# Kernel tuning notes

Measured on AMD Instinct MI355X. Metric: run time of the kernel, lower is better.

## Reference

```python
import jax, jax.numpy as jnp
import numpy as np

B, N, D, E = 4, 16384, 128, 1048576  # batch, nodes/graph, hidden, total edges


def setup_inputs() -> dict:
    key = jax.random.key(0)
    k0, k1, k2, k3, k4, k5, k6 = jax.random.split(key, 7)
    x = jax.random.normal(k0, (B, N, D), dtype=jnp.float32)
    W = jax.random.normal(k1, (D, D), dtype=jnp.float32) * 0.05  # 'random_normal' init
    b = jax.random.normal(k2, (D,), dtype=jnp.float32) * 0.05
    edge_b = jax.random.randint(k3, (E,), 0, B, dtype=jnp.int32)
    edge_row = jax.random.randint(k4, (E,), 0, N, dtype=jnp.int32)
    edge_col = jax.random.randint(k5, (E,), 0, N, dtype=jnp.int32)
    edge_vals = jax.random.uniform(k6, (E,), dtype=jnp.float32)
    return {"x": x, "W": W, "b": b, "edge_b": edge_b, "edge_row": edge_row,
            "edge_col": edge_col, "edge_vals": edge_vals, "k": 2}


def reference(x, W, b, edge_b, edge_row, edge_col, edge_vals, k):
    # adj is a batched sparse [B, N, N]; edges stored as (batch, row, col, val) COO.
    seg_row = edge_b * N + edge_row  # flattened destination id in [0, B*N)
    # in_degrees = sum_j |adj[b, i, j]|
    deg = jax.ops.segment_sum(jnp.abs(edge_vals), seg_row, num_segments=B * N)
    deg = deg.reshape(B, N)
    norm = jnp.power(deg + 1e-6, -0.5)[..., None]          # [B, N, 1]
    norm_k = jnp.power(norm, k)                             # computed but unused (faithful to source)
    support = jnp.einsum('bnd,de->bne', x, W)               # x @ W
    y = (support * norm).reshape(B * N, D)                  # pre-normalized features
    # SpMM: out[b, i] = sum_{(b,i,j)} adj_val * y[b, j]
    msgs = y[edge_b * N + edge_col] * edge_vals[:, None]    # [E, D] gather + scale
    agg = jax.ops.segment_sum(msgs, seg_row, num_segments=B * N).reshape(B, N, D)
    return jax.nn.relu(agg * norm + b)
```

## Files before the change

kernel.cpp:

```cpp
#include <hip/hip_runtime.h>
#include <stdint.h>

#define B_ 4
#define N_ 16384
#define D_ 128
#define E_ 1048576
#define BN_ 65536
#define NBKT 256
#define NBLK 256
#define CAP  6144
#define CAPQ 1536

typedef __attribute__((ext_vector_type(8))) short short8;
typedef __attribute__((ext_vector_type(4))) float floatx4;

static constexpr size_t OFF_Y      = 0;
static constexpr size_t OFF_PACK1  = 16777216;
static constexpr size_t OFF_GBKT   = OFF_PACK1 + 12582912;
static constexpr size_t OFF_NORM   = OFF_GBKT + 1024;
static constexpr size_t OFF_ROWST  = OFF_NORM + 262144;
static constexpr size_t OFF_WH     = OFF_ROWST + 262144;
static constexpr size_t OFF_WL     = OFF_WH + 32768;

__device__ __forceinline__ uint32_t rne16(uint32_t u) {
    return (u + 0x7FFFu + ((u >> 16) & 1u)) >> 16;
}
__device__ __forceinline__ void bf16split(float f, uint16_t& h, uint16_t& l) {
    uint32_t hb = rne16(__float_as_uint(f));
    h = (uint16_t)hb;
    float r = f - __uint_as_float(hb << 16);
    l = (uint16_t)rne16(__float_as_uint(r));
}

__global__ __launch_bounds__(1024, 2) void k_scatter(const int* __restrict__ eb,
                                                     const int* __restrict__ er,
                                                     const int* __restrict__ ec,
                                                     const float* __restrict__ ev,
                                                     const float* __restrict__ Wg,
                                                     uint32_t* __restrict__ gbkt,
                                                     uint2* __restrict__ pack1,
                                                     uint16_t* __restrict__ WhG,
                                                     uint16_t* __restrict__ WlG) {
    __shared__ uint32_t h[NBKT];
    int t = threadIdx.x;
    if (t < NBKT) h[t] = 0;
    if (blockIdx.x < 16) {
        int g = blockIdx.x * 1024 + t;
        float w = Wg[g];
        uint16_t hh, ll;
        bf16split(w, hh, ll);
        int k = g >> 7, n = g & 127;
        int o = ((k >> 3) * 128 + n) * 8 + (k & 7);
        WhG[o] = hh;
        WlG[o] = ll;
    }
    __syncthreads();
    int vbase = blockIdx.x * 1024 + t;
    int4   b4 = ((const int4*)eb)[vbase];
    int4   r4 = ((const int4*)er)[vbase];
    int4   c4 = ((const int4*)ec)[vbase];
    float4 v4 = ((const float4*)ev)[vbase];
    uint32_t k0 = (uint32_t)(b4.x * N_ + r4.x);
    uint32_t k1 = (uint32_t)(b4.y * N_ + r4.y);
    uint32_t k2 = (uint32_t)(b4.z * N_ + r4.z);
    uint32_t k3 = (uint32_t)(b4.w * N_ + r4.w);
    atomicAdd(&h[k0 >> 8], 1u);
    atomicAdd(&h[k1 >> 8], 1u);
    atomicAdd(&h[k2 >> 8], 1u);
    atomicAdd(&h[k3 >> 8], 1u);
    __syncthreads();
    if (t < NBKT) {
        uint32_t c = h[t];
        uint32_t base = c ? atomicAdd(&gbkt[t], c) : 0u;
        h[t] = base;
    }
    __syncthreads();
    {
        uint32_t off = atomicAdd(&h[k0 >> 8], 1u);
        pack1[(size_t)(k0 >> 8) * CAP + off] =
            make_uint2(((k0 & 255u) << 14) | (uint32_t)c4.x, __float_as_uint(v4.x));
    }
    {
        uint32_t off = atomicAdd(&h[k1 >> 8], 1u);
        pack1[(size_t)(k1 >> 8) * CAP + off] =
            make_uint2(((k1 & 255u) << 14) | (uint32_t)c4.y, __float_as_uint(v4.y));
    }
    {
        uint32_t off = atomicAdd(&h[k2 >> 8], 1u);
        pack1[(size_t)(k2 >> 8) * CAP + off] =
            make_uint2(((k2 & 255u) << 14) | (uint32_t)c4.z, __float_as_uint(v4.z));
    }
    {
        uint32_t off = atomicAdd(&h[k3 >> 8], 1u);
        pack1[(size_t)(k3 >> 8) * CAP + off] =
            make_uint2(((k3 & 255u) << 14) | (uint32_t)c4.w, __float_as_uint(v4.w));
    }
}

__global__ __launch_bounds__(1024) void k_degsort(const uint32_t* __restrict__ gbkt,
                                                  const uint2* __restrict__ pack1,
                                                  float* __restrict__ norm,
                                                  uint32_t* __restrict__ rowst) {
    __shared__ float    dsum[NBKT];
    __shared__ uint32_t cnt[NBKT];
    __shared__ uint32_t scn[NBKT];
    int t = threadIdx.x;
    int bkt = blockIdx.x;
    if (t < NBKT) { dsum[t] = 0.f; cnt[t] = 0; }
    __syncthreads();
    uint32_t n = gbkt[bkt];
    size_t bstart = (size_t)bkt * CAP;
    for (uint32_t i = t; i < n; i += 1024) {
        uint2 p = pack1[bstart + i];
        uint32_t nl = p.x >> 14;
        atomicAdd(&cnt[nl], 1u);
        atomicAdd(&dsum[nl], fabsf(__uint_as_float(p.y)));
    }
    __syncthreads();
    if (t < NBKT) scn[t] = cnt[t];
    __syncthreads();
    for (int off = 1; off < NBKT; off <<= 1) {
        uint32_t a = 0;
        if (t < NBKT && t >= off) a = scn[t - off];
        __syncthreads();
        if (t < NBKT) scn[t] += a;
        __syncthreads();
    }
    if (t < NBKT) {
        norm[bkt * NBKT + t] = rsqrtf(dsum[t] + 1e-6f);
        rowst[bkt * NBKT + t] = scn[t] - cnt[t];
    }
}

__global__ __launch_bounds__(256) void k_matmul_mfma(const float* __restrict__ x,
                                                     const uint16_t* __restrict__ WhG,
                                                     const uint16_t* __restrict__ WlG,
                                                     const float* __restrict__ norm,
                                                     uint32_t* __restrict__ ybf) {
    __shared__ short WhS[16384];
    __shared__ short WlS[16384];
    __shared__ short XhS[4096];
    __shared__ short XlS[4096];
    __shared__ float normS[32];
    int tid = threadIdx.x;
    int row0 = blockIdx.x * 32;

    {
        const uint4* whg = (const uint4*)WhG;
        const uint4* wlg = (const uint4*)WlG;
        uint4* whs = (uint4*)WhS;
        uint4* wls = (uint4*)WlS;
#pragma unroll
        for (int i = 0; i < 8; ++i) {
            whs[i * 256 + tid] = whg[i * 256 + tid];
            wls[i * 256 + tid] = wlg[i * 256 + tid];
        }
    }
#pragma unroll
    for (int cc = 0; cc < 2; ++cc) {
        int c = cc * 256 + tid;
        int m = c & 31, kk = c >> 5;
        const float4* xp = (const float4*)(x + (size_t)(row0 + m) * D_ + kk * 8);
        float4 f0 = xp[0], f1 = xp[1];
        union { short8 v; uint16_t s[8]; } uh, ul;
        bf16split(f0.x, uh.s[0], ul.s[0]); bf16split(f0.y, uh.s[1], ul.s[1]);
        bf16split(f0.z, uh.s[2], ul.s[2]); bf16split(f0.w, uh.s[3], ul.s[3]);
        bf16split(f1.x, uh.s[4], ul.s[4]); bf16split(f1.y, uh.s[5], ul.s[5]);
        bf16split(f1.z, uh.s[6], ul.s[6]); bf16split(f1.w, uh.s[7], ul.s[7]);
        ((short8*)XhS)[c] = uh.v;
        ((short8*)XlS)[c] = ul.v;
    }
    if (tid < 32) normS[tid] = norm[row0 + tid];
    __syncthreads();

    int lane = tid & 63;
    int wv = tid >> 6;
    int quad = lane >> 4;
    int l15 = lane & 15;
    int wcol0 = wv * 32;
    floatx4 acc[2][2] = {};
    const short8* Xh8 = (const short8*)XhS;
    const short8* Xl8 = (const short8*)XlS;
    const short8* Wh8 = (const short8*)WhS;
    const short8* Wl8 = (const short8*)WlS;
#pragma unroll
    for (int ks = 0; ks < 4; ++ks) {
        int kkq = ks * 4 + quad;
        short8 ah0 = Xh8[kkq * 32 + l15];
        short8 ah1 = Xh8[kkq * 32 + 16 + l15];
        short8 al0 = Xl8[kkq * 32 + l15];
        short8 al1 = Xl8[kkq * 32 + 16 + l15];
        short8 bh0 = Wh8[kkq * 128 + wcol0 + l15];
        short8 bh1 = Wh8[kkq * 128 + wcol0 + 16 + l15];
        short8 bl0 = Wl8[kkq * 128 + wcol0 + l15];
        short8 bl1 = Wl8[kkq * 128 + wcol0 + 16 + l15];
        acc[0][0] = __builtin_amdgcn_mfma_f32_16x16x32_bf16(ah0, bh0, acc[0][0], 0, 0, 0);
        acc[0][1] = __builtin_amdgcn_mfma_f32_16x16x32_bf16(ah0, bh1, acc[0][1], 0, 0, 0);
        acc[1][0] = __builtin_amdgcn_mfma_f32_16x16x32_bf16(ah1, bh0, acc[1][0], 0, 0, 0);
        acc[1][1] = __builtin_amdgcn_mfma_f32_16x16x32_bf16(ah1, bh1, acc[1][1], 0, 0, 0);
        acc[0][0] = __builtin_amdgcn_mfma_f32_16x16x32_bf16(ah0, bl0, acc[0][0], 0, 0, 0);
        acc[0][1] = __builtin_amdgcn_mfma_f32_16x16x32_bf16(ah0, bl1, acc[0][1], 0, 0, 0);
        acc[1][0] = __builtin_amdgcn_mfma_f32_16x16x32_bf16(ah1, bl0, acc[1][0], 0, 0, 0);
        acc[1][1] = __builtin_amdgcn_mfma_f32_16x16x32_bf16(ah1, bl1, acc[1][1], 0, 0, 0);
        acc[0][0] = __builtin_amdgcn_mfma_f32_16x16x32_bf16(al0, bh0, acc[0][0], 0, 0, 0);
        acc[0][1] = __builtin_amdgcn_mfma_f32_16x16x32_bf16(al0, bh1, acc[0][1], 0, 0, 0);
        acc[1][0] = __builtin_amdgcn_mfma_f32_16x16x32_bf16(al1, bh0, acc[1][0], 0, 0, 0);
        acc[1][1] = __builtin_amdgcn_mfma_f32_16x16x32_bf16(al1, bh1, acc[1][1], 0, 0, 0);
    }

#pragma unroll
    for (int rt = 0; rt < 2; ++rt) {
#pragma unroll
        for (int ct = 0; ct < 2; ++ct) {
            floatx4 v = acc[rt][ct];
            int rbase = rt * 16 + quad * 4;
            int cp = (wcol0 + ct * 16) / 2 + (l15 >> 1);
#pragma unroll
            for (int r = 0; r < 4; ++r) {
                float mine = v[r] * normS[rbase + r];
                float oth = __shfl_xor(mine, 1, 64);
                uint32_t a = __float_as_uint((lane & 1) ? oth : mine);
                uint32_t b = __float_as_uint((lane & 1) ? mine : oth);
                uint32_t packed = rne16(a) | (rne16(b) << 16);
                bool doit = ((lane & 1) == 0) ? (r < 2) : (r >= 2);
                if (doit)
                    ybf[(size_t)(row0 + rbase + r) * 64 + cp] = packed;
            }
        }
    }
}

__device__ __forceinline__ void fma8(float* acc, float v, uint4 u) {
    acc[0] = fmaf(v, __uint_as_float(u.x << 16), acc[0]);
    acc[1] = fmaf(v, __uint_as_float(u.x & 0xFFFF0000u), acc[1]);
    acc[2] = fmaf(v, __uint_as_float(u.y << 16), acc[2]);
    acc[3] = fmaf(v, __uint_as_float(u.y & 0xFFFF0000u), acc[3]);
    acc[4] = fmaf(v, __uint_as_float(u.z << 16), acc[4]);
    acc[5] = fmaf(v, __uint_as_float(u.z & 0xFFFF0000u), acc[5]);
    acc[6] = fmaf(v, __uint_as_float(u.w << 16), acc[6]);
    acc[7] = fmaf(v, __uint_as_float(u.w & 0xFFFF0000u), acc[7]);
}

__global__ __launch_bounds__(512, 8) void k_spmm(const uint32_t* __restrict__ gbkt,
                                                 const uint2* __restrict__ pack1,
                                                 const uint32_t* __restrict__ rowst,
                                                 const uint4* __restrict__ y4,
                                                 const float* __restrict__ norm,
                                                 const float* __restrict__ bias,
                                                 float* __restrict__ out) {
    __shared__ uint2    srt[CAPQ];
    __shared__ uint32_t rs[65];
    __shared__ uint32_t rcur[64];
    int t = threadIdx.x;
    int blk = blockIdx.x;
    int xcd = blk & 7;
    int batch = xcd & 3;
    int qhi = xcd >> 2;
    int j = blk >> 3;
    int quarter = qhi * 2 + (j & 1);
    int bkt = batch * 64 + (j >> 1);
    int nbase = quarter * 64;
    uint32_t n = gbkt[bkt];
    if (t < 64) { rs[t] = rowst[bkt * NBKT + nbase + t]; rcur[t] = 0; }
    if (t == 64) rs[64] = (quarter == 3) ? n : rowst[bkt * NBKT + nbase + 64];
    __syncthreads();
    uint32_t qbase = rs[0];
    size_t base = (size_t)bkt * CAP;
    for (uint32_t i = t; i < n; i += 512) {
        uint2 p = pack1[base + i];
        uint32_t nl = p.x >> 14;
        if ((int)(nl >> 6) == quarter) {
            uint32_t loc = nl & 63;
            uint32_t pos = rs[loc] - qbase + atomicAdd(&rcur[loc], 1u);
            srt[pos] = p;
        }
    }
    __syncthreads();

    int wv = t >> 6;
    int lane = t & 63;
    int esub = lane >> 4;
    int chunk = lane & 15;
    uint32_t colbase = (uint32_t)batch << 14;
#pragma unroll 1
    for (int i = 0; i < 8; ++i) {
        int nl = wv * 8 + i;
        uint32_t e = rs[nl] - qbase;
        uint32_t end = rs[nl + 1] - qbase;
        float acc[8] = {0.f,0.f,0.f,0.f,0.f,0.f,0.f,0.f};
        for (; e + 16 <= end; e += 16) {
            uint2 pa = srt[e + esub];
            uint2 pb = srt[e + 4 + esub];
            uint2 pc = srt[e + 8 + esub];
            uint2 pd = srt[e + 12 + esub];
            uint4 ua = y4[(size_t)(colbase | (pa.x & 0x3FFFu)) * 16 + chunk];
            uint4 ub = y4[(size_t)(colbase | (pb.x & 0x3FFFu)) * 16 + chunk];
            uint4 uc = y4[(size_t)(colbase | (pc.x & 0x3FFFu)) * 16 + chunk];
            uint4 ud = y4[(size_t)(colbase | (pd.x & 0x3FFFu)) * 16 + chunk];
            fma8(acc, __uint_as_float(pa.y), ua);
            fma8(acc, __uint_as_float(pb.y), ub);
            fma8(acc, __uint_as_float(pc.y), uc);
            fma8(acc, __uint_as_float(pd.y), ud);
        }
        for (; e + 4 <= end; e += 4) {
            uint2 p = srt[e + esub];
            uint4 u = y4[(size_t)(colbase | (p.x & 0x3FFFu)) * 16 + chunk];
            fma8(acc, __uint_as_float(p.y), u);
        }
        if (e < end) {
            uint32_t idx = e + esub;
            bool act = idx < end;
            uint2 p = srt[act ? idx : (end - 1)];
            uint4 u = y4[(size_t)(colbase | (p.x & 0x3FFFu)) * 16 + chunk];
            float v = act ? __uint_as_float(p.y) : 0.f;
            fma8(acc, v, u);
        }
#pragma unroll
        for (int jj = 0; jj < 8; ++jj) {
            acc[jj] += __shfl_xor(acc[jj], 16, 64);
            acc[jj] += __shfl_xor(acc[jj], 32, 64);
        }
        if (esub < 2) {
            int node = bkt * NBKT + nbase + nl;
            float nm = norm[node];
            float4 bb = ((const float4*)bias)[chunk * 2 + esub];
            float4 o;
            o.x = fmaxf(fmaf(acc[esub * 4 + 0], nm, bb.x), 0.f);
            o.y = fmaxf(fmaf(acc[esub * 4 + 1], nm, bb.y), 0.f);
            o.z = fmaxf(fmaf(acc[esub * 4 + 2], nm, bb.z), 0.f);
            o.w = fmaxf(fmaf(acc[esub * 4 + 3], nm, bb.w), 0.f);
            ((float4*)out)[(size_t)node * 32 + chunk * 2 + esub] = o;
        }
    }
}

extern "C" void kernel_launch(void* const* d_in, const int* in_sizes, int n_in,
                              void* d_out, int out_size, void* d_ws, size_t ws_size,
                              hipStream_t stream) {
    const float* x  = (const float*)d_in[0];
    const float* W  = (const float*)d_in[1];
    const float* bi = (const float*)d_in[2];
    const int* eb   = (const int*)d_in[3];
    const int* er   = (const int*)d_in[4];
    const int* ec   = (const int*)d_in[5];
    const float* ev = (const float*)d_in[6];
    float* out = (float*)d_out;

    char* ws = (char*)d_ws;
    uint32_t* ybf    = (uint32_t*)(ws + OFF_Y);
    uint2*    pack1  = (uint2*)(ws + OFF_PACK1);
    uint32_t* gbkt   = (uint32_t*)(ws + OFF_GBKT);
    float*    norm   = (float*)(ws + OFF_NORM);
    uint32_t* rowst  = (uint32_t*)(ws + OFF_ROWST);
    uint16_t* WhG    = (uint16_t*)(ws + OFF_WH);
    uint16_t* WlG    = (uint16_t*)(ws + OFF_WL);

    hipMemsetAsync(gbkt, 0, NBKT * sizeof(uint32_t), stream);
    k_scatter<<<NBLK, 1024, 0, stream>>>(eb, er, ec, ev, W, gbkt, pack1, WhG, WlG);
    k_degsort<<<NBKT, 1024, 0, stream>>>(gbkt, pack1, norm, rowst);
    k_matmul_mfma<<<BN_ / 32, 256, 0, stream>>>(x, WhG, WlG, norm, ybf);
    k_spmm   <<<1024, 512, 0, stream>>>(gbkt, pack1, rowst, (const uint4*)ybf, norm, bi, out);
}
```

Measured before the change: 181.3 us.

## Sort edges by row once in degsort and read sorted edges globally in SpMM

The per-row counting sort of each bucket's edges moves into the degree kernel, which stages it in LDS (48KB) and writes the sorted bucket back to global memory in place. The SpMM kernel no longer rescans the whole bucket four times, once per quarter block, to build an LDS-sorted copy. It reads edges straight from global memory at the row offsets. This removes redundant global reads and LDS atomics in SpMM and shrinks its LDS use, which may raise occupancy. In exchange, edge reads in the inner loop become global loads instead of LDS loads, and degsort does an extra read and write pass. Bounds checks against CAP are also added.

```diff
diff --git a/kernel.cpp b/kernel.cpp
--- a/kernel.cpp
+++ b/kernel.cpp
@@ -9,7 +9,6 @@
 #define NBKT 256
 #define NBLK 256
 #define CAP  6144
-#define CAPQ 1536
 
 typedef __attribute__((ext_vector_type(8))) short short8;
 typedef __attribute__((ext_vector_type(4))) float floatx4;
@@ -77,38 +76,45 @@
     __syncthreads();
     {
         uint32_t off = atomicAdd(&h[k0 >> 8], 1u);
-        pack1[(size_t)(k0 >> 8) * CAP + off] =
-            make_uint2(((k0 & 255u) << 14) | (uint32_t)c4.x, __float_as_uint(v4.x));
+        if (off < CAP)
+            pack1[(size_t)(k0 >> 8) * CAP + off] =
+                make_uint2(((k0 & 255u) << 14) | (uint32_t)c4.x, __float_as_uint(v4.x));
     }
     {
         uint32_t off = atomicAdd(&h[k1 >> 8], 1u);
-        pack1[(size_t)(k1 >> 8) * CAP + off] =
-            make_uint2(((k1 & 255u) << 14) | (uint32_t)c4.y, __float_as_uint(v4.y));
+        if (off < CAP)
+            pack1[(size_t)(k1 >> 8) * CAP + off] =
+                make_uint2(((k1 & 255u) << 14) | (uint32_t)c4.y, __float_as_uint(v4.y));
     }
     {
         uint32_t off = atomicAdd(&h[k2 >> 8], 1u);
-        pack1[(size_t)(k2 >> 8) * CAP + off] =
-            make_uint2(((k2 & 255u) << 14) | (uint32_t)c4.z, __float_as_uint(v4.z));
+        if (off < CAP)
+            pack1[(size_t)(k2 >> 8) * CAP + off] =
+                make_uint2(((k2 & 255u) << 14) | (uint32_t)c4.z, __float_as_uint(v4.z));
     }
     {
         uint32_t off = atomicAdd(&h[k3 >> 8], 1u);
-        pack1[(size_t)(k3 >> 8) * CAP + off] =
-            make_uint2(((k3 & 255u) << 14) | (uint32_t)c4.w, __float_as_uint(v4.w));
+        if (off < CAP)
+            pack1[(size_t)(k3 >> 8) * CAP + off] =
+                make_uint2(((k3 & 255u) << 14) | (uint32_t)c4.w, __float_as_uint(v4.w));
     }
 }
 
 __global__ __launch_bounds__(1024) void k_degsort(const uint32_t* __restrict__ gbkt,
-                                                  const uint2* __restrict__ pack1,
+                                                  uint2* __restrict__ pack1,
                                                   float* __restrict__ norm,
                                                   uint32_t* __restrict__ rowst) {
+    __shared__ uint2    sE[CAP];
     __shared__ float    dsum[NBKT];
     __shared__ uint32_t cnt[NBKT];
     __shared__ uint32_t scn[NBKT];
+    __shared__ uint32_t cur[NBKT];
     int t = threadIdx.x;
     int bkt = blockIdx.x;
     if (t < NBKT) { dsum[t] = 0.f; cnt[t] = 0; }
     __syncthreads();
     uint32_t n = gbkt[bkt];
+    if (n > CAP) n = CAP;
     size_t bstart = (size_t)bkt * CAP;
     for (uint32_t i = t; i < n; i += 1024) {
         uint2 p = pack1[bstart + i];
@@ -128,8 +134,20 @@
     }
     if (t < NBKT) {
         norm[bkt * NBKT + t] = rsqrtf(dsum[t] + 1e-6f);
-        rowst[bkt * NBKT + t] = scn[t] - cnt[t];
-    }
+        uint32_t st = scn[t] - cnt[t];
+        rowst[bkt * NBKT + t] = st;
+        cur[t] = st;
+    }
+    __syncthreads();
+    for (uint32_t i = t; i < n; i += 1024) {
+        uint2 p = pack1[bstart + i];
+        uint32_t nl = p.x >> 14;
+        uint32_t pos = atomicAdd(&cur[nl], 1u);
+        if (pos < CAP) sE[pos] = p;
+    }
+    __syncthreads();
+    for (uint32_t i = t; i < n; i += 1024)
+        pack1[bstart + i] = sE[i];
 }
 
 __global__ __launch_bounds__(256) void k_matmul_mfma(const float* __restrict__ x,
@@ -248,9 +266,7 @@
                                                  const float* __restrict__ norm,
                                                  const float* __restrict__ bias,
                                                  float* __restrict__ out) {
-    __shared__ uint2    srt[CAPQ];
     __shared__ uint32_t rs[65];
-    __shared__ uint32_t rcur[64];
     int t = threadIdx.x;
     int blk = blockIdx.x;
     int xcd = blk & 7;
@@ -261,21 +277,11 @@
     int bkt = batch * 64 + (j >> 1);
     int nbase = quarter * 64;
     uint32_t n = gbkt[bkt];
-    if (t < 64) { rs[t] = rowst[bkt * NBKT + nbase + t]; rcur[t] = 0; }
+    if (n > CAP) n = CAP;
+    if (t < 64) rs[t] = rowst[bkt * NBKT + nbase + t];
     if (t == 64) rs[64] = (quarter == 3) ? n : rowst[bkt * NBKT + nbase + 64];
     __syncthreads();
-    uint32_t qbase = rs[0];
-    size_t base = (size_t)bkt * CAP;
-    for (uint32_t i = t; i < n; i += 512) {
-        uint2 p = pack1[base + i];
-        uint32_t nl = p.x >> 14;
-        if ((int)(nl >> 6) == quarter) {
-            uint32_t loc = nl & 63;
-            uint32_t pos = rs[loc] - qbase + atomicAdd(&rcur[loc], 1u);
-            srt[pos] = p;
-        }
-    }
-    __syncthreads();
+    const uint2* eptr = pack1 + (size_t)bkt * CAP;
 
     int wv = t >> 6;
     int lane = t & 63;
@@ -285,14 +291,14 @@
 #pragma unroll 1
     for (int i = 0; i < 8; ++i) {
         int nl = wv * 8 + i;
-        uint32_t e = rs[nl] - qbase;
-        uint32_t end = rs[nl + 1] - qbase;
+        uint32_t e = rs[nl];
+        uint32_t end = rs[nl + 1];
         float acc[8] = {0.f,0.f,0.f,0.f,0.f,0.f,0.f,0.f};
         for (; e + 16 <= end; e += 16) {
-            uint2 pa = srt[e + esub];
-            uint2 pb = srt[e + 4 + esub];
-            uint2 pc = srt[e + 8 + esub];
-            uint2 pd = srt[e + 12 + esub];
+            uint2 pa = eptr[e + esub];
+            uint2 pb = eptr[e + 4 + esub];
+            uint2 pc = eptr[e + 8 + esub];
+            uint2 pd = eptr[e + 12 + esub];
             uint4 ua = y4[(size_t)(colbase | (pa.x & 0x3FFFu)) * 16 + chunk];
             uint4 ub = y4[(size_t)(colbase | (pb.x & 0x3FFFu)) * 16 + chunk];
             uint4 uc = y4[(size_t)(colbase | (pc.x & 0x3FFFu)) * 16 + chunk];
@@ -303,14 +309,14 @@
             fma8(acc, __uint_as_float(pd.y), ud);
         }
         for (; e + 4 <= end; e += 4) {
-            uint2 p = srt[e + esub];
+            uint2 p = eptr[e + esub];
             uint4 u = y4[(size_t)(colbase | (p.x & 0x3FFFu)) * 16 + chunk];
             fma8(acc, __uint_as_float(p.y), u);
         }
         if (e < end) {
             uint32_t idx = e + esub;
             bool act = idx < end;
-            uint2 p = srt[act ? idx : (end - 1)];
+            uint2 p = eptr[act ? idx : (end - 1)];
             uint4 u = y4[(size_t)(colbase | (p.x & 0x3FFFu)) * 16 + chunk];
             float v = act ? __uint_as_float(p.y) : 0.f;
             fma8(acc, v, u);
```

Result: no change. 179.2 us (-1.1%).
